# Optimization experiments

Hardware: AMD Instinct MI355X
Metric: run time of the kernel (lower is better)

## Reference

```python
import jax, jax.numpy as jnp
import numpy as np
import math

B, L, D_IN, H, N, N_CLASSES = 16, 8192, 128, 256, 64, 10
DT_MIN, DT_MAX = 1e-3, 1e-1


def setup_inputs() -> dict:
    key = jax.random.key(0)
    ks = jax.random.split(key, 16)
    x = jax.random.normal(ks[0], (B, L, D_IN), dtype=jnp.float32)
    # fc1
    W1 = jax.random.normal(ks[1], (D_IN, H), dtype=jnp.float32) / np.sqrt(D_IN)
    b1 = jnp.zeros((H,), jnp.float32)
    # LayerNorm
    ln_g = jnp.ones((H,), jnp.float32)
    ln_b = jnp.zeros((H,), jnp.float32)
    # S4D kernel params (standard S4D-Lin init)
    log_dt = jax.random.uniform(ks[2], (H,), jnp.float32) * (
        math.log(DT_MAX) - math.log(DT_MIN)) + math.log(DT_MIN)
    log_A_real = jnp.log(0.5 * jnp.ones((H, N // 2), jnp.float32))
    A_imag = math.pi * jnp.broadcast_to(jnp.arange(N // 2, dtype=jnp.float32), (H, N // 2))
    C_re = jax.random.normal(ks[3], (H, N // 2), dtype=jnp.float32)
    C_im = jax.random.normal(ks[4], (H, N // 2), dtype=jnp.float32)
    Dp = jax.random.normal(ks[5], (H,), dtype=jnp.float32)
    # output_linear: Conv1d(H, 2H, 1) + GLU
    Wo = jax.random.normal(ks[6], (H, 2 * H), dtype=jnp.float32) / np.sqrt(H)
    bo = jnp.zeros((2 * H,), jnp.float32)
    # head
    W2 = jax.random.normal(ks[7], (H, 512), dtype=jnp.float32) / np.sqrt(H)
    b2 = jnp.zeros((512,), jnp.float32)
    W3 = jax.random.normal(ks[8], (512, N_CLASSES), dtype=jnp.float32) / np.sqrt(512)
    b3 = jnp.zeros((N_CLASSES,), jnp.float32)
    return dict(x=x, W1=W1, b1=b1, ln_g=ln_g, ln_b=ln_b, log_dt=log_dt,
                log_A_real=log_A_real, A_imag=A_imag, C_re=C_re, C_im=C_im,
                Dp=Dp, Wo=Wo, bo=bo, W2=W2, b2=b2, W3=W3, b3=b3)


def _s4d_kernel(log_dt, log_A_real, A_imag, C_re, C_im, length):
    dt = jnp.exp(log_dt)[:, None]                       # (H,1)
    A = -jnp.exp(log_A_real) + 1j * A_imag               # (H,N/2) complex
    dtA = A * dt                                          # (H,N/2)
    C = (C_re + 1j * C_im) * (jnp.exp(dtA) - 1.0) / A     # (H,N/2)
    l = jnp.arange(length, dtype=jnp.float32)
    vand = jnp.exp(dtA[:, :, None] * l)                   # (H,N/2,L) Vandermonde
    return 2.0 * jnp.einsum('hn,hnl->hl', C, vand).real   # (H,L)


def reference(x, W1, b1, ln_g, ln_b, log_dt, log_A_real, A_imag, C_re, C_im,
              Dp, Wo, bo, W2, b2, W3, b3):
    # fc1 + ReLU
    h = jax.nn.relu(x @ W1 + b1)                          # (B,L,H)
    # LayerNorm
    mu = jnp.mean(h, axis=-1, keepdims=True)
    var = jnp.mean(jnp.square(h - mu), axis=-1, keepdims=True)
    u = (h - mu) * jax.lax.rsqrt(var + 1e-5) * ln_g + ln_b
    # S4D: FFT long convolution along L
    Lseq = u.shape[1]
    k = _s4d_kernel(log_dt, log_A_real, A_imag, C_re, C_im, Lseq)  # (H,L)
    n_fft = 2 * Lseq
    k_f = jnp.fft.rfft(k, n=n_fft, axis=-1)               # (H,F)
    u_f = jnp.fft.rfft(u, n=n_fft, axis=1)                # (B,F,H)
    y = jnp.fft.irfft(u_f * k_f.T[None], n=n_fft, axis=1)[:, :Lseq]  # (B,L,H)
    y = y + u * Dp                                        # skip D term
    y = jax.nn.gelu(y, approximate=False)
    # output_linear: pointwise conv to 2H + GLU
    v = y @ Wo + bo                                       # (B,L,2H)
    y = v[..., :H] * jax.nn.sigmoid(v[..., H:])           # GLU
    # max-pool over sequence
    pooled = jnp.max(y, axis=1)                           # (B,H)
    f = jax.nn.leaky_relu(pooled @ W2 + b2, negative_slope=0.01)
    logits = f @ W3 + b3                                  # (B,n_classes)
    Y_hat = jnp.argmax(logits, axis=0)                    # matches torch dim=0
    return logits, Y_hat
```

## Files before the change

kernel.cpp:

```cpp
#include <hip/hip_runtime.h>
#include <math.h>

typedef float f32x4 __attribute__((ext_vector_type(4)));
typedef short bf16x8 __attribute__((ext_vector_type(8)));

#define BB 16
#define LL 8192
#define DIN 128
#define HH 256
#define NCH 32
#define TCH 256

#define U_OFF    0ull
#define PRM_OFF  67108864ull
#define KK_OFF   67371008ull
#define WKE_OFF  67633152ull
#define F_OFF    109576192ull
#define SB_OFF   117964800ull
#define SBH_OFF  134742016ull
#define W1T_OFF  151519232ull
#define WOT_OFF  151584768ull
#define PART_OFF 151846912ull
#define POOL_OFF 152895488ull
#define FC_OFF   152911872ull

static __device__ __forceinline__ unsigned short f2b(float f){
  unsigned int u = __float_as_uint(f);
  return (unsigned short)((u + 0x7fffu + ((u>>16)&1u)) >> 16);
}
static __device__ __forceinline__ float b2f(unsigned int h){
  return __uint_as_float((h & 0xffffu)<<16);
}

static __device__ __forceinline__ float gelu_t(float v){
  float vv = v*v;
  float p  = fmaf(0.044715f, vv, 1.0f);
  float z  = v*p*(-1.5957691216057308f);
  float e  = __expf(z);
  return v*__builtin_amdgcn_rcpf(1.0f + e);
}

typedef __attribute__((address_space(3))) unsigned int lds_u32_t;
typedef const __attribute__((address_space(1))) unsigned int glb_u32_t;
static __device__ __forceinline__ void gl16(const void* g, void* l){
  __builtin_amdgcn_global_load_lds((glb_u32_t*)g, (lds_u32_t*)l, 16, 0, 0);
}

__global__ void k0_params(const float* __restrict__ log_dt, const float* __restrict__ log_A_real,
                          const float* __restrict__ A_imag, const float* __restrict__ C_re,
                          const float* __restrict__ C_im, float* __restrict__ prm){
  int id = blockIdx.x*256 + threadIdx.x;
  if (id >= 8192) return;
  int h = id >> 5;
  float dt = expf(log_dt[h]);
  float Ar = -expf(log_A_real[id]);
  float Ai = A_imag[id];
  float dr = Ar*dt, di = Ai*dt;
  float ear = expf(dr);
  float are = ear*cosf(di), aim = ear*sinf(di);
  float er = are - 1.0f, ei = aim;
  float den = 1.0f/(Ar*Ar + Ai*Ai);
  float Br = (er*Ar + ei*Ai)*den;
  float Bi = (ei*Ar - er*Ai)*den;
  float c_r = C_re[id], c_i = C_im[id];
  float cre = 2.0f*(c_r*Br - c_i*Bi);
  float cim = 2.0f*(c_r*Bi + c_i*Br);
  double phi = (double)di*(double)TCH;
  float eT = expf(dr*(float)TCH);
  float aTre = eT*(float)cos(phi);
  float aTim = eT*(float)sin(phi);
  prm[id]         = are;  prm[8192  + id] = aim;
  prm[16384 + id] = cre;  prm[24576 + id] = cim;
  prm[32768 + id] = aTre; prm[40960 + id] = aTim;
  prm[49152 + id] = dr;   prm[57344 + id] = di;
}

__global__ void kp_ker(const float* __restrict__ prm, float* __restrict__ kker){
  int id = blockIdx.x*256 + threadIdx.x;
  int h = id >> 8, d = id & 255;
  float fd = (float)d;
  float s = 0.f;
  #pragma unroll 8
  for (int n = 0; n < 32; ++n){
    int i0 = (h<<5) + n;
    float dr = prm[49152 + i0], di = prm[57344 + i0];
    float cr = prm[16384 + i0], ci = prm[24576 + i0];
    float e = expf(dr*fd);
    float ph = di*fd;
    s += e*(cr*cosf(ph) - ci*sinf(ph));
  }
  kker[id] = s;
}

__global__ void kp_ef(const float* __restrict__ prm, unsigned short* __restrict__ wke,
                      unsigned short* __restrict__ fb){
  int id = blockIdx.x*256 + threadIdx.x;
  int h = id >> 5, n = id & 31;
  float ar = prm[id], ai = prm[8192+id], cr = prm[16384+id], ci = prm[24576+id];
  int q = 32 + (n >> 2);
  int c = (n & 3) << 1;
  unsigned short* W = wke + (size_t)h*81920 + ((size_t)q<<11) + c;
  float zr = cr, zi = ci;
  for (int m = 0; m < 256; ++m){
    float t1 = zr*ar - zi*ai, t2 = zr*ai + zi*ar;
    zr = t1; zi = t2;
    *(unsigned int*)(W + (m<<3)) = ((unsigned int)f2b(-zi)<<16) | f2b(zr);
  }
  unsigned short* Fh = fb + ((size_t)h<<14) + (n<<9);
  float wr_ = 1.f, wi_ = 0.f;
  Fh[255] = f2b(1.f); Fh[256+255] = f2b(0.f);
  for (int j = 254; j >= 0; --j){
    float t1 = wr_*ar - wi_*ai, t2 = wr_*ai + wi_*ar;
    wr_ = t1; wi_ = t2;
    Fh[j] = f2b(wr_); Fh[256+j] = f2b(wi_);
  }
}

__global__ void kp_wke(const float* __restrict__ kker, const float* __restrict__ Dp,
                       unsigned short* __restrict__ wke){
  int id = blockIdx.x*256 + threadIdx.x;
  int h = id >> 8, m = id & 255;
  const float* kh = kker + (h<<8);
  float dp = Dp[h];
  unsigned short* W = wke + (size_t)h*81920;
  for (int j4 = 0; j4 < 256; j4 += 4){
    ushort4 o;
    float v0 = (j4+0 <= m) ? kh[m-j4-0] : 0.f; if (j4+0 == m) v0 += dp;
    float v1 = (j4+1 <= m) ? kh[m-j4-1] : 0.f; if (j4+1 == m) v1 += dp;
    float v2 = (j4+2 <= m) ? kh[m-j4-2] : 0.f; if (j4+2 == m) v2 += dp;
    float v3 = (j4+3 <= m) ? kh[m-j4-3] : 0.f; if (j4+3 == m) v3 += dp;
    o.x = f2b(v0); o.y = f2b(v1); o.z = f2b(v2); o.w = f2b(v3);
    *(ushort4*)(W + (((j4>>3)<<11)) + (m<<3) + (j4&7)) = o;
  }
}

__global__ void kw_wot(const float* __restrict__ Wo, unsigned short* __restrict__ wot){
  int id = blockIdx.x*256 + threadIdx.x;
  int k = id >> 9, n = id & 511;
  wot[n*256 + k] = f2b(Wo[id]);
}
__global__ void kw_w1t(const float* __restrict__ W1, unsigned short* __restrict__ w1t){
  int id = blockIdx.x*256 + threadIdx.x;
  int k = id >> 8, n = id & 255;
  w1t[((k>>3)<<11) + (n<<3) + (k&7)] = f2b(W1[k*256 + n]);
}

__global__ __launch_bounds__(512, 4) void k1_fc1_ln(const float* __restrict__ x,
    const unsigned short* __restrict__ w1t, const float* __restrict__ b1,
    const float* __restrict__ lng, const float* __restrict__ lnb,
    unsigned short* __restrict__ u){
  __shared__ unsigned short sX[64*128];
  __shared__ float sRed[4][64][2];
  int t = threadIdx.x;
  int lane = t & 63, wid = t >> 6;
  int wr = wid >> 2, wc = wid & 3;
  int g0 = blockIdx.x << 6;
  int b = g0 >> 13, l0 = g0 & 8191;
  {
    int r = t >> 3, kq = (t & 7) << 4;
    const float* xr = x + (size_t)(g0 + r)*DIN + kq;
    #pragma unroll
    for (int i = 0; i < 4; ++i){
      float4 v = *(const float4*)(xr + i*4);
      ushort4 o; o.x=f2b(v.x); o.y=f2b(v.y); o.z=f2b(v.z); o.w=f2b(v.w);
      int k0 = kq + i*4;
      int q = k0 >> 3;
      *(ushort4*)&sX[(r<<7) + ((q ^ (r&7))<<3) + (k0&7)] = o;
    }
  }
  __syncthreads();
  f32x4 acc[2][4];
  #pragma unroll
  for (int mi = 0; mi < 2; ++mi)
    #pragma unroll
    for (int ni = 0; ni < 4; ++ni) acc[mi][ni] = (f32x4){0.f,0.f,0.f,0.f};
  #pragma unroll
  for (int kt = 0; kt < 4; ++kt){
    bf16x8 af[2];
    #pragma unroll
    for (int mi = 0; mi < 2; ++mi){
      int m = (wr<<5) + (mi<<4) + (lane&15);
      int q = (kt<<2) + (lane>>4);
      af[mi] = *(const bf16x8*)&sX[(m<<7) + ((q ^ (m&7))<<3)];
    }
    #pragma unroll
    for (int ni = 0; ni < 4; ++ni){
      int hcol = (wc<<6) + (ni<<4) + (lane&15);
      bf16x8 bf = *(const bf16x8*)(w1t + (((kt<<2) + (lane>>4))<<11) + (hcol<<3));
      acc[0][ni] = __builtin_amdgcn_mfma_f32_16x16x32_bf16(af[0], bf, acc[0][ni], 0,0,0);
      acc[1][ni] = __builtin_amdgcn_mfma_f32_16x16x32_bf16(af[1], bf, acc[1][ni], 0,0,0);
    }
  }
  float bv[4];
  #pragma unroll
  for (int ni = 0; ni < 4; ++ni) bv[ni] = b1[(wc<<6) + (ni<<4) + (lane&15)];
  float s1[2][4] = {{0,0,0,0},{0,0,0,0}}, s2[2][4] = {{0,0,0,0},{0,0,0,0}};
  #pragma unroll
  for (int mi = 0; mi < 2; ++mi)
    #pragma unroll
    for (int ni = 0; ni < 4; ++ni)
      #pragma unroll
      for (int rr = 0; rr < 4; ++rr){
        float v = acc[mi][ni][rr] + bv[ni];
        v = v > 0.f ? v : 0.f;
        acc[mi][ni][rr] = v;
        s1[mi][rr] += v; s2[mi][rr] = fmaf(v, v, s2[mi][rr]);
      }
  #pragma unroll
  for (int off = 1; off < 16; off <<= 1)
    #pragma unroll
    for (int mi = 0; mi < 2; ++mi)
      #pragma unroll
      for (int rr = 0; rr < 4; ++rr){
        s1[mi][rr] += __shfl_xor(s1[mi][rr], off);
        s2[mi][rr] += __shfl_xor(s2[mi][rr], off);
      }
  if ((lane & 15) == 0){
    #pragma unroll
    for (int mi = 0; mi < 2; ++mi)
      #pragma unroll
      for (int rr = 0; rr < 4; ++rr){
        int row = (wr<<5) + (mi<<4) + ((lane>>4)<<2) + rr;
        sRed[wc][row][0] = s1[mi][rr];
        sRed[wc][row][1] = s2[mi][rr];
      }
  }
  __syncthreads();
  float mu[2][4], rs[2][4];
  #pragma unroll
  for (int mi = 0; mi < 2; ++mi)
    #pragma unroll
    for (int rr = 0; rr < 4; ++rr){
      int row = (wr<<5) + (mi<<4) + ((lane>>4)<<2) + rr;
      float t1 = sRed[0][row][0] + sRed[1][row][0] + sRed[2][row][0] + sRed[3][row][0];
      float t2 = sRed[0][row][1] + sRed[1][row][1] + sRed[2][row][1] + sRed[3][row][1];
      float m_ = t1*(1.f/256.f);
      mu[mi][rr] = m_;
      rs[mi][rr] = rsqrtf(t2*(1.f/256.f) - m_*m_ + 1e-5f);
    }
  #pragma unroll
  for (int ni = 0; ni < 4; ++ni){
    int hcol = (wc<<6) + (ni<<4) + (lane&15);
    float g = lng[hcol], bb = lnb[hcol];
    #pragma unroll
    for (int mi = 0; mi < 2; ++mi){
      ushort4 o;
      o.x = f2b((acc[mi][ni][0]-mu[mi][0])*rs[mi][0]*g + bb);
      o.y = f2b((acc[mi][ni][1]-mu[mi][1])*rs[mi][1]*g + bb);
      o.z = f2b((acc[mi][ni][2]-mu[mi][2])*rs[mi][2]*g + bb);
      o.w = f2b((acc[mi][ni][3]-mu[mi][3])*rs[mi][3]*g + bb);
      *(ushort4*)(u + (((size_t)(b*HH + hcol))<<13) + l0 + (wr<<5) + (mi<<4) + ((lane>>4)<<2)) = o;
    }
  }
}

__global__ __launch_bounds__(256, 4) void k2a_states(const unsigned short* __restrict__ u,
                                                     const unsigned short* __restrict__ fb,
                                                     unsigned short* __restrict__ sbuf){
  __shared__ unsigned short sA2[2][64*32];
  __shared__ unsigned short sB2[2][128*32];
  int bid = blockIdx.x;
  int lb = ((bid & 7) << 7) + (bid >> 3);
  int h = lb >> 2, nt = lb & 3;
  int t = threadIdx.x;
  int lane = t & 63, wid = t >> 6;
  int wr = wid >> 1, wc = wid & 1;

  int ar0 = t >> 2;
  int asl = t & 3;
  int asw = (asl ^ ((ar0 >> 1) & 3)) << 3;
  const unsigned short* aS = fb + ((size_t)h<<14) + ar0*256 + asw;

  int lcol = t >> 2;
  int bsl  = t & 3;
  int bsw  = (bsl ^ ((lcol >> 1) & 3)) << 3;
  int bc0  = (nt << 7) + lcol;
  int bc1  = bc0 + 64;
  const unsigned short* bS0 = u + (((size_t)((bc0>>5)*HH + h)) << 13) + ((bc0&31) << 8) + bsw;
  const unsigned short* bS1 = u + (((size_t)((bc1>>5)*HH + h)) << 13) + ((bc1&31) << 8) + bsw;

  unsigned short* dA[2]  = { &sA2[0][wid<<9], &sA2[1][wid<<9] };
  unsigned short* dB0[2] = { &sB2[0][wid<<9], &sB2[1][wid<<9] };
  unsigned short* dB1[2] = { &sB2[0][2048 + (wid<<9)], &sB2[1][2048 + (wid<<9)] };

  int aoff[2], boff[4];
  #pragma unroll
  for (int mi = 0; mi < 2; ++mi){
    int m = (wr<<5) + (mi<<4) + (lane&15);
    aoff[mi] = (m<<5) + (((lane>>4) ^ ((m>>1)&3))<<3);
  }
  #pragma unroll
  for (int ni = 0; ni < 4; ++ni){
    int c = (wc<<6) + (ni<<4) + (lane&15);
    boff[ni] = (c<<5) + (((lane>>4) ^ ((c>>1)&3))<<3);
  }

  f32x4 acc[2][4];
  #pragma unroll
  for (int mi = 0; mi < 2; ++mi)
    #pragma unroll
    for (int ni = 0; ni < 4; ++ni) acc[mi][ni] = (f32x4){0.f,0.f,0.f,0.f};

  gl16(aS, dA[0]);
  gl16(bS0, dB0[0]);
  gl16(bS1, dB1[0]);
  __syncthreads();

  #pragma unroll 2
  for (int kt = 0; kt < 8; ++kt){
    int cur = kt & 1;
    if (kt < 7){
      int k1o = (kt+1) << 5;
      gl16(aS  + k1o, dA[cur^1]);
      gl16(bS0 + k1o, dB0[cur^1]);
      gl16(bS1 + k1o, dB1[cur^1]);
    }
    const unsigned short* Ab = sA2[cur];
    const unsigned short* Bb = sB2[cur];
    bf16x8 af[2], bfv[4];
    #pragma unroll
    for (int mi = 0; mi < 2; ++mi) af[mi] = *(const bf16x8*)(Ab + aoff[mi]);
    #pragma unroll
    for (int ni = 0; ni < 4; ++ni) bfv[ni] = *(const bf16x8*)(Bb + boff[ni]);
    #pragma unroll
    for (int mi = 0; mi < 2; ++mi)
      #pragma unroll
      for (int ni = 0; ni < 4; ++ni)
        acc[mi][ni] = __builtin_amdgcn_mfma_f32_16x16x32_bf16(af[mi], bfv[ni], acc[mi][ni], 0,0,0);
    __syncthreads();
  }

  unsigned short* bS[4];
  #pragma unroll
  for (int ni = 0; ni < 4; ++ni){
    int bc = (nt<<7) + (wc<<6) + (ni<<4) + (lane&15);
    bS[ni] = sbuf + (((size_t)(bc>>5)*HH + h)*NCH + (bc&31))*64;
  }
  #pragma unroll
  for (int ni = 0; ni < 4; ++ni)
    #pragma unroll
    for (int mi = 0; mi < 2; ++mi){
      int srow = (wr<<5) + (mi<<4) + ((lane>>4)<<2);
      ushort4 o;
      o.x = f2b(acc[mi][ni][0]); o.y = f2b(acc[mi][ni][1]);
      o.z = f2b(acc[mi][ni][2]); o.w = f2b(acc[mi][ni][3]);
      *(ushort4*)(bS[ni] + srow) = o;
    }
}

__global__ void k2b_scan(const float* __restrict__ prm, const unsigned short* __restrict__ sbuf,
                         unsigned short* __restrict__ sbh){
  int tid = blockIdx.x*512 + threadIdx.x;
  int n = tid & 31, h = (tid >> 5) & 255, b = tid >> 13;
  int i0 = (h<<5) + n;
  float aTr = prm[32768 + i0], aTi = prm[40960 + i0];
  size_t base = (((size_t)b*HH + h)*NCH)*64 + (n<<1);
  float ir = 0.f, ii = 0.f;
  for (int c = 0; c < NCH; ++c){
    size_t o = base + (size_t)(c<<6);
    *(unsigned int*)(sbh + o) = ((unsigned int)f2b(ii)<<16) | f2b(ir);
    unsigned int rw = *(const unsigned int*)(sbuf + o);
    float lr = b2f(rw), li = b2f(rw>>16);
    float nr = fmaf(aTr, ir, fmaf(-aTi, ii, lr));
    float ni_ = fmaf(aTr, ii, fmaf(aTi, ir, li));
    ir = nr; ii = ni_;
  }
}

__global__ __launch_bounds__(512, 4) void k2c_emit(unsigned short* __restrict__ uy,
                                                   const unsigned short* __restrict__ wke,
                                                   const unsigned short* __restrict__ sbh){
  __shared__ unsigned short sB[2][128*32];
  __shared__ unsigned short sW[8][1152];
  int bid = blockIdx.x;
  int lb = ((bid & 7) << 7) + (bid >> 3);
  int h = lb >> 2, nt = lb & 3;
  int t = threadIdx.x;
  int lane = t & 63, wid = t >> 6;
  int wr = wid >> 1, wc = wid & 1;

  const unsigned short* wkeh = wke + (size_t)h*81920;

  int bcol = t >> 2;
  int bsl  = t & 3;
  int bsw  = (bsl ^ ((bcol >> 1) & 3)) << 3;
  int bcg  = (nt << 7) + bcol;
  int bb   = bcg >> 5, chk = bcg & 31;
  const unsigned short* bSU = uy  + (((size_t)(bb*HH + h)) << 13) + (chk << 8) + bsw;
  const unsigned short* bSS = sbh + (((size_t)bb*HH + h)*NCH + chk)*64 + bsw;

  unsigned short* dB0 = &sB[0][wid<<9];
  unsigned short* dB0b= &sB[1][wid<<9];

  int am[4];
  #pragma unroll
  for (int mi = 0; mi < 4; ++mi) am[mi] = (wr<<6) + (mi<<4) + (lane&15);
  int boff[4];
  #pragma unroll
  for (int ni = 0; ni < 4; ++ni){
    int c = (wc<<6) + (ni<<4) + (lane&15);
    boff[ni] = (c<<5) + (((lane>>4) ^ ((c>>1)&3))<<3);
  }

  f32x4 acc[4][4];
  #pragma unroll
  for (int mi = 0; mi < 4; ++mi)
    #pragma unroll
    for (int ni = 0; ni < 4; ++ni) acc[mi][ni] = (f32x4){0.f,0.f,0.f,0.f};

  gl16(bSU, dB0);
  __syncthreads();

  #pragma unroll 2
  for (int kt = 0; kt < 10; ++kt){
    int cur = kt & 1;
    if (kt < 9){
      int k1o = (kt+1) << 5;
      const unsigned short* bs = (kt+1 < 8) ? (bSU + k1o) : (bSS + ((kt+1-8) << 5));
      gl16(bs, cur ? dB0 : dB0b);
    }
    int q = (kt<<2) + (lane>>4);
    const unsigned short* Ab = wkeh + ((size_t)q<<11);
    const unsigned short* Bb = sB[cur];
    bf16x8 af[4], bfv[4];
    #pragma unroll
    for (int mi = 0; mi < 4; ++mi) af[mi] = *(const bf16x8*)(Ab + (am[mi]<<3));
    #pragma unroll
    for (int ni = 0; ni < 4; ++ni) bfv[ni] = *(const bf16x8*)(Bb + boff[ni]);
    #pragma unroll
    for (int mi = 0; mi < 4; ++mi)
      #pragma unroll
      for (int ni = 0; ni < 4; ++ni)
        acc[mi][ni] = __builtin_amdgcn_mfma_f32_16x16x32_bf16(af[mi], bfv[ni], acc[mi][ni], 0,0,0);
    __syncthreads();
  }

  unsigned short* wbase = sW[wid];
  int col16 = lane & 15;
  int rcol  = lane >> 2;
  int rseg  = lane & 3;
  #pragma unroll
  for (int ni = 0; ni < 4; ++ni){
    #pragma unroll
    for (int mi = 0; mi < 4; ++mi){
      int mloc = (mi<<4) + ((lane>>4)<<2);
      ushort4 o;
      #pragma unroll
      for (int rr = 0; rr < 4; ++rr)
        ((unsigned short*)&o)[rr] = f2b(gelu_t(acc[mi][ni][rr]));
      *(ushort4*)&wbase[col16*72 + mloc] = o;
    }
    int bcO = (nt<<7) + (wc<<6) + (ni<<4) + rcol;
    unsigned short* op = uy + (((size_t)((bcO>>5)*HH + h))<<13) + ((bcO&31)<<8)
                       + (wr<<6) + (rseg<<4);
    uint4 va = *(const uint4*)&wbase[rcol*72 + (rseg<<4)];
    uint4 vb = *(const uint4*)&wbase[rcol*72 + (rseg<<4) + 8];
    *(uint4*)op       = va;
    *(uint4*)(op + 8) = vb;
  }
}

__global__ __launch_bounds__(512) void k3_glu(const unsigned short* __restrict__ y,
                                              const unsigned short* __restrict__ wot,
                                              const float* __restrict__ bo,
                                              float* __restrict__ part){
  __shared__ unsigned short sA[128*64];
  __shared__ unsigned short sB[2][128*64];
  __shared__ float smax[2][256];
  int t = threadIdx.x;
  int lane = t & 63, wid = t >> 6;
  int wg = wid >> 2;
  int wl = wid & 3;
  int bid = blockIdx.x;
  int lb = ((bid & 7) << 8) + (bid >> 3);
  int js2 = lb & 1, mb = (lb >> 1) & 63, b = lb >> 7;
  int js = (js2 << 1) + wg;
  f32x4 acc[2][8];
  #pragma unroll
  for (int i = 0; i < 2; ++i)
    #pragma unroll
    for (int j = 0; j < 8; ++j)
      acc[i][j] = (f32x4){0.f,0.f,0.f,0.f};

  for (int kt = 0; kt < 4; ++kt){
    __syncthreads();
    {
      int hl = t & 63, g = t >> 6;
      const unsigned short* yb = y + (((size_t)(b*HH + (kt<<6) + hl))<<13) + (mb<<7);
      int qh = hl >> 3, hm = hl & 7;
      #pragma unroll
      for (int rep = 0; rep < 2; ++rep){
        int m0 = ((rep<<3) + g) << 3;
        float4 v = *(const float4*)(yb + m0);
        const unsigned short* pv = (const unsigned short*)&v;
        #pragma unroll
        for (int j = 0; j < 8; ++j){
          int m = m0 + j;
          sA[(m<<6) + ((qh ^ (m&7))<<3) + hm] = pv[j];
        }
      }
    }
    {
      int tt = t & 255;
      #pragma unroll
      for (int p = 0; p < 4; ++p){
        int idx = (p<<8) + tt;
        int row = idx >> 3, sl = idx & 7;
        int ng = (row < 64) ? ((js<<6) + row) : (256 + (js<<6) + row - 64);
        const float4 v = *(const float4*)(wot + (ng<<8) + (kt<<6) + (sl<<3));
        *(float4*)&sB[wg][(row<<6) + ((sl ^ (row&7))<<3)] = v;
      }
    }
    __syncthreads();
    #pragma unroll
    for (int kk = 0; kk < 2; ++kk){
      bf16x8 af[2], bfr[8];
      #pragma unroll
      for (int mi = 0; mi < 2; ++mi){
        int r = (wl<<5) + (mi<<4) + (lane&15);
        int sl = (kk<<2) + (lane>>4);
        af[mi] = *(const bf16x8*)&sA[(r<<6) + ((sl ^ (r&7))<<3)];
      }
      #pragma unroll
      for (int ni = 0; ni < 8; ++ni){
        int r = (ni<<4) + (lane&15);
        int sl = (kk<<2) + (lane>>4);
        bfr[ni] = *(const bf16x8*)&sB[wg][(r<<6) + ((sl ^ (r&7))<<3)];
      }
      #pragma unroll
      for (int ni = 0; ni < 8; ++ni)
        #pragma unroll
        for (int mi = 0; mi < 2; ++mi)
          acc[mi][ni] = __builtin_amdgcn_mfma_f32_16x16x32_bf16(af[mi], bfr[ni], acc[mi][ni], 0, 0, 0);
    }
  }

  float bo1[4], bo2[4];
  #pragma unroll
  for (int ni = 0; ni < 4; ++ni){
    int col = (js<<6) + (ni<<4) + (lane&15);
    bo1[ni] = bo[col]; bo2[ni] = bo[256 + col];
  }
  #pragma unroll
  for (int ni = 0; ni < 4; ++ni){
    float m = -3.4e38f;
    #pragma unroll
    for (int mi = 0; mi < 2; ++mi)
      #pragma unroll
      for (int r = 0; r < 4; ++r){
        float v1 = acc[mi][ni][r] + bo1[ni];
        float v2 = acc[mi][ni+4][r] + bo2[ni];
        float g = v1 * (1.0f/(1.0f + __expf(-v2)));
        m = fmaxf(m, g);
      }
    m = fmaxf(m, __shfl_xor(m, 16));
    m = fmaxf(m, __shfl_xor(m, 32));
    if (lane < 16) smax[wg][(wl<<6) + (ni<<4) + lane] = m;
  }
  __syncthreads();
  if (t < 128){
    int wg2 = t >> 6, tt = t & 63;
    int jso = (js2 << 1) + wg2;
    float m = fmaxf(fmaxf(smax[wg2][tt], smax[wg2][64+tt]),
                    fmaxf(smax[wg2][128+tt], smax[wg2][192+tt]));
    part[(((size_t)b<<6) + mb)*256 + (jso<<6) + tt] = m;
  }
}

__global__ void k35_pool(const float* __restrict__ part, float* __restrict__ pool){
  int b = blockIdx.x, j = threadIdx.x;
  float m = -3.4e38f;
  for (int mb = 0; mb < 64; ++mb)
    m = fmaxf(m, part[(((size_t)b<<6) + mb)*256 + j]);
  pool[(b<<8) + j] = m;
}
__global__ void k4a_fc2(const float* __restrict__ pool, const float* __restrict__ W2,
                        const float* __restrict__ b2, float* __restrict__ f){
  int id = blockIdx.x*256 + threadIdx.x;
  int b = id >> 9, ko = id & 511;
  float s = b2[ko];
  #pragma unroll 8
  for (int hh = 0; hh < 256; ++hh)
    s = fmaf(pool[(b<<8) + hh], W2[hh*512 + ko], s);
  f[id] = s > 0.0f ? s : 0.01f*s;
}
__global__ void k4b_head(const float* __restrict__ f, const float* __restrict__ W3,
                         const float* __restrict__ b3, float* __restrict__ out){
  __shared__ float lg[160];
  int t = threadIdx.x;
  if (t < 160){
    int b = t/10, c = t - 10*b;
    float s = b3[c];
    #pragma unroll 8
    for (int ko = 0; ko < 512; ++ko)
      s = fmaf(f[(b<<9) + ko], W3[ko*10 + c], s);
    lg[t] = s;
    out[t] = s;
  }
  __syncthreads();
  if (t < 10){
    int bi = 0; float bvv = lg[t];
    for (int b2i = 1; b2i < 16; ++b2i){
      float vv = lg[b2i*10 + t];
      if (vv > bvv){ bvv = vv; bi = b2i; }
    }
    out[160 + t] = (float)bi;
  }
}

extern "C" void kernel_launch(void* const* d_in, const int* in_sizes, int n_in,
                              void* d_out, int out_size, void* d_ws, size_t ws_size,
                              hipStream_t stream) {
  const float* x      = (const float*)d_in[0];
  const float* W1     = (const float*)d_in[1];
  const float* b1     = (const float*)d_in[2];
  const float* lng    = (const float*)d_in[3];
  const float* lnb    = (const float*)d_in[4];
  const float* log_dt = (const float*)d_in[5];
  const float* logA   = (const float*)d_in[6];
  const float* Aim    = (const float*)d_in[7];
  const float* Cre    = (const float*)d_in[8];
  const float* Cim    = (const float*)d_in[9];
  const float* Dp     = (const float*)d_in[10];
  const float* Wo     = (const float*)d_in[11];
  const float* bo     = (const float*)d_in[12];
  const float* W2     = (const float*)d_in[13];
  const float* b2     = (const float*)d_in[14];
  const float* W3     = (const float*)d_in[15];
  const float* b3     = (const float*)d_in[16];
  char* wsb = (char*)d_ws;
  unsigned short* u   = (unsigned short*)(wsb + U_OFF);
  float* prm          = (float*)(wsb + PRM_OFF);
  float* kker         = (float*)(wsb + KK_OFF);
  unsigned short* wke = (unsigned short*)(wsb + WKE_OFF);
  unsigned short* fb  = (unsigned short*)(wsb + F_OFF);
  unsigned short* sb  = (unsigned short*)(wsb + SB_OFF);
  unsigned short* sbh = (unsigned short*)(wsb + SBH_OFF);
  unsigned short* w1t = (unsigned short*)(wsb + W1T_OFF);
  unsigned short* wot = (unsigned short*)(wsb + WOT_OFF);
  float* part         = (float*)(wsb + PART_OFF);
  float* pool         = (float*)(wsb + POOL_OFF);
  float* fbuf         = (float*)(wsb + FC_OFF);
  float* out          = (float*)d_out;

  k0_params<<<dim3(32),   dim3(256), 0, stream>>>(log_dt, logA, Aim, Cre, Cim, prm);
  kp_ker   <<<dim3(256),  dim3(256), 0, stream>>>(prm, kker);
  kp_ef    <<<dim3(32),   dim3(256), 0, stream>>>(prm, wke, fb);
  kp_wke   <<<dim3(256),  dim3(256), 0, stream>>>(kker, Dp, wke);
  kw_wot   <<<dim3(512),  dim3(256), 0, stream>>>(Wo, wot);
  kw_w1t   <<<dim3(128),  dim3(256), 0, stream>>>(W1, w1t);
  k1_fc1_ln<<<dim3(2048), dim3(512), 0, stream>>>(x, w1t, b1, lng, lnb, u);
  k2a_states<<<dim3(1024),dim3(256), 0, stream>>>(u, fb, sb);
  k2b_scan <<<dim3(256),  dim3(512), 0, stream>>>(prm, sb, sbh);
  k2c_emit <<<dim3(1024), dim3(512), 0, stream>>>(u, wke, sbh);
  k3_glu   <<<dim3(2048), dim3(512), 0, stream>>>(u, wot, bo, part);
  k35_pool <<<dim3(16),   dim3(256), 0, stream>>>(part, pool);
  k4a_fc2  <<<dim3(32),   dim3(256), 0, stream>>>(pool, W2, b2, fbuf);
  k4b_head <<<dim3(1),    dim3(256), 0, stream>>>(fbuf, W3, b3, out);
}
```

Measured before the change: 299.1 us.

## Merge parameter-prep kernels and replace serial power recurrences with closed-form exp/sincos

After: 251.0 us. 1.19x faster.

```diff
diff --git a/kernel.cpp b/kernel.cpp
--- a/kernel.cpp
+++ b/kernel.cpp
@@ -46,81 +46,120 @@
   __builtin_amdgcn_global_load_lds((glb_u32_t*)g, (lds_u32_t*)l, 16, 0, 0);
 }
 
-__global__ void k0_params(const float* __restrict__ log_dt, const float* __restrict__ log_A_real,
-                          const float* __restrict__ A_imag, const float* __restrict__ C_re,
-                          const float* __restrict__ C_im, float* __restrict__ prm){
-  int id = blockIdx.x*256 + threadIdx.x;
-  if (id >= 8192) return;
-  int h = id >> 5;
-  float dt = expf(log_dt[h]);
-  float Ar = -expf(log_A_real[id]);
-  float Ai = A_imag[id];
-  float dr = Ar*dt, di = Ai*dt;
-  float ear = expf(dr);
-  float are = ear*cosf(di), aim = ear*sinf(di);
-  float er = are - 1.0f, ei = aim;
-  float den = 1.0f/(Ar*Ar + Ai*Ai);
-  float Br = (er*Ar + ei*Ai)*den;
-  float Bi = (ei*Ar - er*Ai)*den;
-  float c_r = C_re[id], c_i = C_im[id];
-  float cre = 2.0f*(c_r*Br - c_i*Bi);
-  float cim = 2.0f*(c_r*Bi + c_i*Br);
-  double phi = (double)di*(double)TCH;
-  float eT = expf(dr*(float)TCH);
-  float aTre = eT*(float)cos(phi);
-  float aTim = eT*(float)sin(phi);
-  prm[id]         = are;  prm[8192  + id] = aim;
-  prm[16384 + id] = cre;  prm[24576 + id] = cim;
-  prm[32768 + id] = aTre; prm[40960 + id] = aTim;
-  prm[49152 + id] = dr;   prm[57344 + id] = di;
-}
-
-__global__ void kp_ker(const float* __restrict__ prm, float* __restrict__ kker){
-  int id = blockIdx.x*256 + threadIdx.x;
-  int h = id >> 8, d = id & 255;
-  float fd = (float)d;
-  float s = 0.f;
-  #pragma unroll 8
-  for (int n = 0; n < 32; ++n){
-    int i0 = (h<<5) + n;
-    float dr = prm[49152 + i0], di = prm[57344 + i0];
-    float cr = prm[16384 + i0], ci = prm[24576 + i0];
-    float e = expf(dr*fd);
-    float ph = di*fd;
-    s += e*(cr*cosf(ph) - ci*sinf(ph));
-  }
-  kker[id] = s;
-}
-
-__global__ void kp_ef(const float* __restrict__ prm, unsigned short* __restrict__ wke,
-                      unsigned short* __restrict__ fb){
-  int id = blockIdx.x*256 + threadIdx.x;
-  int h = id >> 5, n = id & 31;
-  float ar = prm[id], ai = prm[8192+id], cr = prm[16384+id], ci = prm[24576+id];
-  int q = 32 + (n >> 2);
-  int c = (n & 3) << 1;
-  unsigned short* W = wke + (size_t)h*81920 + ((size_t)q<<11) + c;
-  float zr = cr, zi = ci;
-  for (int m = 0; m < 256; ++m){
-    float t1 = zr*ar - zi*ai, t2 = zr*ai + zi*ar;
-    zr = t1; zi = t2;
-    *(unsigned int*)(W + (m<<3)) = ((unsigned int)f2b(-zi)<<16) | f2b(zr);
-  }
-  unsigned short* Fh = fb + ((size_t)h<<14) + (n<<9);
-  float wr_ = 1.f, wi_ = 0.f;
-  Fh[255] = f2b(1.f); Fh[256+255] = f2b(0.f);
-  for (int j = 254; j >= 0; --j){
-    float t1 = wr_*ar - wi_*ai, t2 = wr_*ai + wi_*ar;
-    wr_ = t1; wi_ = t2;
-    Fh[j] = f2b(wr_); Fh[256+j] = f2b(wi_);
-  }
-}
-
-__global__ void kp_wke(const float* __restrict__ kker, const float* __restrict__ Dp,
-                       unsigned short* __restrict__ wke){
-  int id = blockIdx.x*256 + threadIdx.x;
-  int h = id >> 8, m = id & 255;
-  const float* kh = kker + (h<<8);
+__global__ __launch_bounds__(256) void kp_all(
+    const float* __restrict__ log_dt, const float* __restrict__ log_A_real,
+    const float* __restrict__ A_imag, const float* __restrict__ C_re,
+    const float* __restrict__ C_im, float* __restrict__ prm,
+    const float* __restrict__ Wo, unsigned short* __restrict__ wot,
+    const float* __restrict__ W1, unsigned short* __restrict__ w1t,
+    unsigned short* __restrict__ wke, unsigned short* __restrict__ fb){
+  int bid = blockIdx.x;
+  int t = threadIdx.x;
+  if (bid < 32){
+    int id = bid*256 + t;
+    int h = id >> 5;
+    float dt = expf(log_dt[h]);
+    float Ar = -expf(log_A_real[id]);
+    float Ai = A_imag[id];
+    float dr = Ar*dt, di = Ai*dt;
+    float ear = expf(dr);
+    float are = ear*cosf(di), aim = ear*sinf(di);
+    float er = are - 1.0f, ei = aim;
+    float den = 1.0f/(Ar*Ar + Ai*Ai);
+    float Br = (er*Ar + ei*Ai)*den;
+    float Bi = (ei*Ar - er*Ai)*den;
+    float c_r = C_re[id], c_i = C_im[id];
+    float cre = 2.0f*(c_r*Br - c_i*Bi);
+    float cim = 2.0f*(c_r*Bi + c_i*Br);
+    double phi = (double)di*(double)TCH;
+    float eT = expf(dr*(float)TCH);
+    float aTre = eT*(float)cos(phi);
+    float aTim = eT*(float)sin(phi);
+    prm[id]         = are;  prm[8192  + id] = aim;
+    prm[16384 + id] = cre;  prm[24576 + id] = cim;
+    prm[32768 + id] = aTre; prm[40960 + id] = aTim;
+    prm[49152 + id] = dr;   prm[57344 + id] = di;
+  } else if (bid < 544){
+    int id = (bid-32)*256 + t;
+    int k = id >> 9, n = id & 511;
+    wot[n*256 + k] = f2b(Wo[id]);
+  } else if (bid < 672){
+    int id = (bid-544)*256 + t;
+    int k = id >> 8, n = id & 255;
+    w1t[((k>>3)<<11) + (n<<3) + (k&7)] = f2b(W1[k*256 + n]);
+  } else if (bid < 2720){
+    int bid2 = bid - 672;
+    int h = bid2 >> 3, ng = bid2 & 7;
+    int nn = t & 3;
+    int n  = (ng<<2) + nn;
+    int hn = (h<<5) + n;
+    float dt = expf(log_dt[h]);
+    float Ar = -expf(log_A_real[hn]);
+    float Ai = A_imag[hn];
+    float dr = Ar*dt, di = Ai*dt;
+    float ear = expf(dr);
+    float are = ear*cosf(di), aim = ear*sinf(di);
+    float er = are - 1.0f, ei = aim;
+    float den = 1.0f/(Ar*Ar + Ai*Ai);
+    float Br = (er*Ar + ei*Ai)*den;
+    float Bi = (ei*Ar - er*Ai)*den;
+    float c_r = C_re[hn], c_i = C_im[hn];
+    float cre = 2.0f*(c_r*Br - c_i*Bi);
+    float cim = 2.0f*(c_r*Bi + c_i*Br);
+    int q = 32 + ng, c = nn << 1;
+    unsigned short* W = wke + (size_t)h*81920 + ((size_t)q<<11) + c;
+    int mb = t >> 2;
+    #pragma unroll
+    for (int i = 0; i < 4; ++i){
+      int m = mb + (i<<6);
+      float fm = (float)(m+1);
+      float E  = expf(dr*fm);
+      float ph = di*fm;
+      float car = E*cosf(ph), sar = E*sinf(ph);
+      float zr = cre*car - cim*sar;
+      float zi = cre*sar + cim*car;
+      *(unsigned int*)(W + (m<<3)) = ((unsigned int)f2b(-zi)<<16) | f2b(zr);
+    }
+  } else {
+    int bid3 = bid - 2720;
+    int h = bid3 >> 5, n = bid3 & 31;
+    int hn = (h<<5) + n;
+    float dt = expf(log_dt[h]);
+    float Ar = -expf(log_A_real[hn]);
+    float Ai = A_imag[hn];
+    float dr = Ar*dt, di = Ai*dt;
+    int j = t;
+    float fp = (float)(255 - j);
+    float E  = expf(dr*fp);
+    float ph = di*fp;
+    unsigned short* Fh = fb + ((size_t)h<<14) + (n<<9);
+    Fh[j]       = f2b(E*cosf(ph));
+    Fh[256 + j] = f2b(E*sinf(ph));
+  }
+}
+
+__global__ __launch_bounds__(256) void kp_khw(const float* __restrict__ prm,
+                                              const float* __restrict__ Dp,
+                                              unsigned short* __restrict__ wke){
+  __shared__ float kh[256];
+  int h = blockIdx.x;
+  int d = threadIdx.x;
+  {
+    float fd = (float)d;
+    float s = 0.f;
+    #pragma unroll 8
+    for (int n = 0; n < 32; ++n){
+      int i0 = (h<<5) + n;
+      float dr = prm[49152 + i0], di = prm[57344 + i0];
+      float cr = prm[16384 + i0], ci = prm[24576 + i0];
+      float e = expf(dr*fd);
+      float ph = di*fd;
+      s += e*(cr*cosf(ph) - ci*sinf(ph));
+    }
+    kh[d] = s;
+  }
+  __syncthreads();
+  int m = threadIdx.x;
   float dp = Dp[h];
   unsigned short* W = wke + (size_t)h*81920;
   for (int j4 = 0; j4 < 256; j4 += 4){
@@ -132,17 +171,6 @@
     o.x = f2b(v0); o.y = f2b(v1); o.z = f2b(v2); o.w = f2b(v3);
     *(ushort4*)(W + (((j4>>3)<<11)) + (m<<3) + (j4&7)) = o;
   }
-}
-
-__global__ void kw_wot(const float* __restrict__ Wo, unsigned short* __restrict__ wot){
-  int id = blockIdx.x*256 + threadIdx.x;
-  int k = id >> 9, n = id & 511;
-  wot[n*256 + k] = f2b(Wo[id]);
-}
-__global__ void kw_w1t(const float* __restrict__ W1, unsigned short* __restrict__ w1t){
-  int id = blockIdx.x*256 + threadIdx.x;
-  int k = id >> 8, n = id & 255;
-  w1t[((k>>3)<<11) + (n<<3) + (k&7)] = f2b(W1[k*256 + n]);
 }
 
 __global__ __launch_bounds__(512, 4) void k1_fc1_ln(const float* __restrict__ x,
@@ -631,7 +659,6 @@
   char* wsb = (char*)d_ws;
   unsigned short* u   = (unsigned short*)(wsb + U_OFF);
   float* prm          = (float*)(wsb + PRM_OFF);
-  float* kker         = (float*)(wsb + KK_OFF);
   unsigned short* wke = (unsigned short*)(wsb + WKE_OFF);
   unsigned short* fb  = (unsigned short*)(wsb + F_OFF);
   unsigned short* sb  = (unsigned short*)(wsb + SB_OFF);
@@ -643,12 +670,9 @@
   float* fbuf         = (float*)(wsb + FC_OFF);
   float* out          = (float*)d_out;
 
-  k0_params<<<dim3(32),   dim3(256), 0, stream>>>(log_dt, logA, Aim, Cre, Cim, prm);
-  kp_ker   <<<dim3(256),  dim3(256), 0, stream>>>(prm, kker);
-  kp_ef    <<<dim3(32),   dim3(256), 0, stream>>>(prm, wke, fb);
-  kp_wke   <<<dim3(256),  dim3(256), 0, stream>>>(kker, Dp, wke);
-  kw_wot   <<<dim3(512),  dim3(256), 0, stream>>>(Wo, wot);
-  kw_w1t   <<<dim3(128),  dim3(256), 0, stream>>>(W1, w1t);
+  kp_all   <<<dim3(10912),dim3(256), 0, stream>>>(log_dt, logA, Aim, Cre, Cim, prm,
+                                                  Wo, wot, W1, w1t, wke, fb);
+  kp_khw   <<<dim3(256),  dim3(256), 0, stream>>>(prm, Dp, wke);
   k1_fc1_ln<<<dim3(2048), dim3(512), 0, stream>>>(x, w1t, b1, lng, lnb, u);
   k2a_states<<<dim3(1024),dim3(256), 0, stream>>>(u, fb, sb);
   k2b_scan <<<dim3(256),  dim3(512), 0, stream>>>(prm, sb, sbh);
```
